# Optimization experiments

Hardware: AMD Instinct MI355X
Metric: run time of the kernel (lower is better)

## Reference

```python
import jax, jax.numpy as jnp
import numpy as np

H = 768
NH = 12
HD = H // NH  # 64
WINDOW = 64  # module's self.window_size; band keeps |i-j| <= WINDOW//2


def setup_inputs() -> dict:
    key = jax.random.key(0)
    ks = jax.random.split(key, 9)
    s = 0.02
    return {
        "hidden_states": jax.random.normal(ks[0], (4, 2048, H), dtype=jnp.float32),
        "Wq": jax.random.normal(ks[1], (H, H), dtype=jnp.float32) * s,
        "bq": jnp.zeros((H,), dtype=jnp.float32),
        "Wk": jax.random.normal(ks[2], (H, H), dtype=jnp.float32) * s,
        "bk": jnp.zeros((H,), dtype=jnp.float32),
        "Wv": jax.random.normal(ks[3], (H, H), dtype=jnp.float32) * s,
        "bv": jnp.zeros((H,), dtype=jnp.float32),
        "Wo": jax.random.normal(ks[4], (H, H), dtype=jnp.float32) * s,
        "bo": jnp.zeros((H,), dtype=jnp.float32),
    }


def _attn(hidden_states, Wq, bq, Wk, bk, Wv, bv, Wo, bo):
    B, S, _ = hidden_states.shape
    # projections (torch Linear uses y = x @ W.T + b; here W is stored already transposed)
    q = (hidden_states @ Wq + bq).reshape(B, S, NH, HD).transpose(0, 2, 1, 3)
    k = (hidden_states @ Wk + bk).reshape(B, S, NH, HD).transpose(0, 2, 1, 3)
    v = (hidden_states @ Wv + bv).reshape(B, S, NH, HD).transpose(0, 2, 1, 3)
    # dense scores [B, NH, S, S], faithful to the original O(S^2) computation
    scores = jnp.einsum("bhqd,bhkd->bhqk", q, k) / jnp.sqrt(jnp.float32(HD))
    # sliding-window band mask: keep j in [i - W//2, i + W//2]
    i = jnp.arange(S)[:, None]
    j = jnp.arange(S)[None, :]
    band = jnp.abs(i - j) <= (WINDOW // 2)
    scores = jnp.where(band[None, None, :, :], scores, jnp.float32(-1e9))
    probs = jax.nn.softmax(scores, axis=-1)
    ctx = jnp.einsum("bhqk,bhkd->bhqd", probs, v)
    ctx = ctx.transpose(0, 2, 1, 3).reshape(B, S, H)
    return ctx @ Wo + bo


def reference(hidden_states, Wq, bq, Wk, bk, Wv, bv, Wo, bo):
    return _attn(hidden_states, Wq, bq, Wk, bk, Wv, bv, Wo, bo)
```

## Files before the change

kernel.cpp:

```cpp
#include <hip/hip_runtime.h>
#include <hip/hip_bf16.h>

#define NHEAD 12
#define HD 64
#define SEQ 2048
#define NB 4
#define HDIM 768
#define MTOT (NB * SEQ)

typedef float f32x4 __attribute__((ext_vector_type(4)));
typedef float f32x16 __attribute__((ext_vector_type(16)));
typedef short s16x8 __attribute__((ext_vector_type(8)));
typedef unsigned short u16x8 __attribute__((ext_vector_type(8)));

__device__ inline unsigned short f2bf(float f) {
    union { float f; unsigned u; } v; v.f = f;
    unsigned r = v.u + 0x7fffu + ((v.u >> 16) & 1u);
    return (unsigned short)(r >> 16);
}
__device__ inline float bf2f(unsigned short u) {
    union { unsigned u; float f; } v; v.u = ((unsigned)u) << 16;
    return v.f;
}
__device__ inline unsigned pack_bf2(float a, float b) {
    return (unsigned)f2bf(a) | ((unsigned)f2bf(b) << 16);
}
__device__ inline s16x8 mk_frag(uint2 lo, uint2 hi) {
    union { unsigned u[4]; s16x8 v; } r;
    r.u[0] = lo.x; r.u[1] = lo.y; r.u[2] = hi.x; r.u[3] = hi.y;
    return r.v;
}

#define MFMA(acc, a, b) \
    acc = __builtin_amdgcn_mfma_f32_16x16x32_bf16((a), (b), (acc), 0, 0, 0)
#define MFMA32(acc, a, b) \
    acc = __builtin_amdgcn_mfma_f32_32x32x16_bf16((a), (b), (acc), 0, 0, 0)

__global__ __launch_bounds__(256) void x_convert(
    const float* __restrict__ X, unsigned short* __restrict__ Xb)
{
    const int i = (blockIdx.x * 256 + threadIdx.x) * 8;
    float4 a = *(const float4*)(X + i);
    float4 b = *(const float4*)(X + i + 4);
    ushort4 wa, wb;
    wa.x = f2bf(a.x); wa.y = f2bf(a.y); wa.z = f2bf(a.z); wa.w = f2bf(a.w);
    wb.x = f2bf(b.x); wb.y = f2bf(b.y); wb.z = f2bf(b.z); wb.w = f2bf(b.w);
    *(ushort4*)(Xb + i) = wa;
    *(ushort4*)(Xb + i + 4) = wb;
}

__global__ __launch_bounds__(256) void w_transpose(
    const float* __restrict__ Wq, const float* __restrict__ Wk,
    const float* __restrict__ Wv, const float* __restrict__ Wo,
    unsigned short* __restrict__ Wt, unsigned short* __restrict__ Wot)
{
    __shared__ __align__(16) unsigned short ts[64][68];
    const int z = blockIdx.z;
    const float* W = (z == 0) ? Wq : (z == 1) ? Wk : (z == 2) ? Wv : Wo;
    unsigned short* D = (z < 3) ? (Wt + (size_t)z * HDIM * HDIM) : Wot;
    const int k0 = blockIdx.x * 64, n0 = blockIdx.y * 64;
    const int t = threadIdx.x;
    const int kr = (t >> 4) * 4;
    const int nc = (t & 15) * 4;
    #pragma unroll
    for (int r = 0; r < 4; r++) {
        float4 v = *(const float4*)(W + (size_t)(k0 + kr + r) * HDIM + n0 + nc);
        ushort4 w;
        w.x = f2bf(v.x); w.y = f2bf(v.y); w.z = f2bf(v.z); w.w = f2bf(v.w);
        *(ushort4*)&ts[kr + r][nc] = w;
    }
    __syncthreads();
    const int nr = t >> 2;
    const int kc = (t & 3) * 16;
    #pragma unroll
    for (int j4 = 0; j4 < 4; j4++) {
        ushort4 w;
        w.x = ts[kc + j4 * 4 + 0][nr];
        w.y = ts[kc + j4 * 4 + 1][nr];
        w.z = ts[kc + j4 * 4 + 2][nr];
        w.w = ts[kc + j4 * 4 + 3][nr];
        *(ushort4*)(D + (size_t)(n0 + nr) * HDIM + k0 + kc + j4 * 4) = w;
    }
}

#define LDP 72

template<int MODE>
__global__ __launch_bounds__(256) void gemm_kernel(
    const unsigned short* __restrict__ A,
    const unsigned short* __restrict__ Bt,
    const float* __restrict__ bias0, const float* __restrict__ bias1,
    const float* __restrict__ bias2,
    unsigned short* __restrict__ Qb, unsigned short* __restrict__ Kb,
    unsigned short* __restrict__ Vb, float* __restrict__ out)
{
    __shared__ __align__(16) unsigned short As[128 * LDP];
    __shared__ __align__(16) unsigned short Bs[128 * LDP];

    const int t = threadIdx.x;
    const int lane = t & 63;
    const int wid = t >> 6;
    const int wm = wid >> 1, wn = wid & 1;
    const int l31 = lane & 31;
    const int lh = lane >> 5;

    const int m0 = blockIdx.y * 128;
    const int n0 = blockIdx.x * 128;

    f32x16 acc[2][2] = {};

    for (int k0 = 0; k0 < HDIM; k0 += 64) {
        u16x8 ra[4], rb[4];
        #pragma unroll
        for (int i = 0; i < 4; i++) {
            const int f = i * 256 + t;
            const int row = f >> 3, c8 = f & 7;
            ra[i] = *(const u16x8*)(A  + (size_t)(m0 + row) * HDIM + k0 + c8 * 8);
            rb[i] = *(const u16x8*)(Bt + (size_t)(n0 + row) * HDIM + k0 + c8 * 8);
        }
        __syncthreads();
        #pragma unroll
        for (int i = 0; i < 4; i++) {
            const int f = i * 256 + t;
            const int row = f >> 3, c8 = f & 7;
            *(u16x8*)(As + row * LDP + c8 * 8) = ra[i];
            *(u16x8*)(Bs + row * LDP + c8 * 8) = rb[i];
        }
        __syncthreads();

        #pragma unroll
        for (int kv = 0; kv < 4; kv++) {
            const int co = kv * 16 + lh * 8;
            s16x8 a0 = *(const s16x8*)(As + (wm * 64 +      l31) * LDP + co);
            s16x8 a1 = *(const s16x8*)(As + (wm * 64 + 32 + l31) * LDP + co);
            s16x8 b0 = *(const s16x8*)(Bs + (wn * 64 +      l31) * LDP + co);
            s16x8 b1 = *(const s16x8*)(Bs + (wn * 64 + 32 + l31) * LDP + co);
            MFMA32(acc[0][0], a0, b0);
            MFMA32(acc[0][1], a0, b1);
            MFMA32(acc[1][0], a1, b0);
            MFMA32(acc[1][1], a1, b1);
        }
    }

    if (MODE == 0) {
        const int z = n0 / HDIM;
        const float* bias = (z == 0) ? bias0 : (z == 1) ? bias1 : bias2;
        const float scale = (z == 0) ? 0.125f : 1.0f;
        unsigned short* dst = (z == 0) ? Qb : (z == 1) ? Kb : Vb;
        #pragma unroll
        for (int fm = 0; fm < 2; fm++) {
            #pragma unroll
            for (int fn = 0; fn < 2; fn++) {
                const int coll = (n0 - z * HDIM) + wn * 64 + fn * 32 + l31;
                const float bc = bias[coll];
                const int h = coll >> 6, d = coll & 63;
                #pragma unroll
                for (int reg = 0; reg < 16; reg++) {
                    const int rowD = (reg & 3) + 8 * (reg >> 2) + 4 * lh;
                    const int m = m0 + wm * 64 + fm * 32 + rowD;
                    const int b = m >> 11, s = m & (SEQ - 1);
                    const size_t idx = (z == 2)
                        ? ((((size_t)b * NHEAD + h) * HD + d) * SEQ + s)
                        : ((((size_t)b * NHEAD + h) * SEQ + s) * HD + d);
                    dst[idx] = f2bf((acc[fm][fn][reg] + bc) * scale);
                }
            }
        }
    } else {
        #pragma unroll
        for (int fm = 0; fm < 2; fm++) {
            #pragma unroll
            for (int fn = 0; fn < 2; fn++) {
                const int col = n0 + wn * 64 + fn * 32 + l31;
                const float bc = bias0[col];
                #pragma unroll
                for (int reg = 0; reg < 16; reg++) {
                    const int rowD = (reg & 3) + 8 * (reg >> 2) + 4 * lh;
                    const int m = m0 + wm * 64 + fm * 32 + rowD;
                    out[(size_t)m * HDIM + col] = acc[fm][fn][reg] + bc;
                }
            }
        }
    }
}

__global__ __launch_bounds__(512) void attn_mfma(
    const unsigned short* __restrict__ Qb, const unsigned short* __restrict__ Kb,
    const unsigned short* __restrict__ Vtg, unsigned short* __restrict__ Cb)
{
    __shared__ __align__(16) unsigned short Ks[192][72];
    __shared__ __align__(16) unsigned short Qs[128][72];
    __shared__ __align__(16) unsigned short Vs[64][208];

    const int t = threadIdx.x;
    const int lane = t & 63;
    const int wq = t >> 6;
    const int woff = wq * 16;
    const int g = lane >> 4, r16 = lane & 15;
    const int q0 = blockIdx.x * 128;
    const int bh = blockIdx.y;
    const int b = bh / NHEAD, h = bh - b * NHEAD;
    const size_t base  = (size_t)bh * SEQ * HD;
    const size_t vbase = (size_t)bh * HD * SEQ;
    const int kstart = q0 - 32;
    const bool interior = (kstart >= 0) && (kstart + 191 < SEQ);

    if (t < 384) {
        const int row = t >> 1, c0 = (t & 1) * 32;
        const int s = kstart + row;
        if (s >= 0 && s < SEQ) {
            const unsigned short* src = Kb + base + (size_t)s * HD + c0;
            #pragma unroll
            for (int j = 0; j < 4; j++)
                *(u16x8*)&Ks[row][c0 + 8 * j] = *(const u16x8*)(src + 8 * j);
        } else {
            const u16x8 z = {};
            #pragma unroll
            for (int j = 0; j < 4; j++)
                *(u16x8*)&Ks[row][c0 + 8 * j] = z;
        }
    }
    {
        const int row = t >> 2, c0 = (t & 3) * 16;
        const unsigned short* src = Qb + base + (size_t)(q0 + row) * HD + c0;
        *(u16x8*)&Qs[row][c0] = *(const u16x8*)src;
        *(u16x8*)&Qs[row][c0 + 8] = *(const u16x8*)(src + 8);
    }
    {
        const int row = t >> 3, c0 = (t & 7) * 24;
        const unsigned short* src = Vtg + vbase + (size_t)row * SEQ + kstart + c0;
        if (interior) {
            #pragma unroll
            for (int j = 0; j < 3; j++)
                *(u16x8*)&Vs[row][c0 + 8 * j] = *(const u16x8*)(src + 8 * j);
        } else {
            for (int e = 0; e < 24; e++) {
                const int s = kstart + c0 + e;
                Vs[row][c0 + e] = (s >= 0 && s < SEQ) ? src[e] : (unsigned short)0;
            }
        }
        if (t < 128) {
            const u16x8 z = {};
            *(u16x8*)&Vs[t >> 1][192 + (t & 1) * 8] = z;
        }
    }
    __syncthreads();

    s16x8 qf[2];
    {
        const unsigned short* p = &Qs[woff + r16][0];
        #pragma unroll
        for (int c = 0; c < 2; c++)
            qf[c] = mk_frag(*(const uint2*)(p + c * 32 + 4 * g),
                            *(const uint2*)(p + c * 32 + 16 + 4 * g));
    }
    f32x4 sacc[5] = {};
    #pragma unroll
    for (int mf = 0; mf < 5; mf++) {
        const unsigned short* p = &Ks[woff + mf * 16 + r16][0];
        #pragma unroll
        for (int c = 0; c < 2; c++) {
            s16x8 kf = mk_frag(*(const uint2*)(p + c * 32 + 4 * g),
                               *(const uint2*)(p + c * 32 + 16 + 4 * g));
            MFMA(sacc[mf], kf, qf[c]);
        }
    }

    float mx = -1e30f;
    #pragma unroll
    for (int mf = 0; mf < 5; mf++) {
        #pragma unroll
        for (int r = 0; r < 4; r++) {
            const int rel = mf * 16 + 4 * g + r - r16;
            const int sg = kstart + woff + mf * 16 + 4 * g + r;
            const bool ok = (rel >= 0) && (rel <= 64) && (sg >= 0) && (sg < SEQ);
            const float v = ok ? sacc[mf][r] : -1e30f;
            sacc[mf][r] = v;
            mx = fmaxf(mx, v);
        }
    }
    mx = fmaxf(mx, __shfl_xor(mx, 16));
    mx = fmaxf(mx, __shfl_xor(mx, 32));
    float l = 0.f;
    #pragma unroll
    for (int mf = 0; mf < 5; mf++) {
        #pragma unroll
        for (int r = 0; r < 4; r++) {
            const float e = __expf(sacc[mf][r] - mx);
            sacc[mf][r] = e;
            l += e;
        }
    }
    l += __shfl_xor(l, 16);
    l += __shfl_xor(l, 32);
    const float inv = 1.f / l;

    s16x8 pf[3];
    #pragma unroll
    for (int c = 0; c < 3; c++) {
        union { unsigned u[4]; s16x8 v; } pv;
        pv.u[0] = pack_bf2(sacc[2 * c][0] * inv, sacc[2 * c][1] * inv);
        pv.u[1] = pack_bf2(sacc[2 * c][2] * inv, sacc[2 * c][3] * inv);
        if (c < 2) {
            pv.u[2] = pack_bf2(sacc[2 * c + 1][0] * inv, sacc[2 * c + 1][1] * inv);
            pv.u[3] = pack_bf2(sacc[2 * c + 1][2] * inv, sacc[2 * c + 1][3] * inv);
        } else {
            pv.u[2] = 0; pv.u[3] = 0;
        }
        pf[c] = pv.v;
    }

    f32x4 cacc[4] = {};
    #pragma unroll
    for (int nf = 0; nf < 4; nf++) {
        const unsigned short* p = &Vs[nf * 16 + r16][woff];
        #pragma unroll
        for (int c = 0; c < 3; c++) {
            s16x8 vf = mk_frag(*(const uint2*)(p + c * 32 + 4 * g),
                               *(const uint2*)(p + c * 32 + 16 + 4 * g));
            MFMA(cacc[nf], pf[c], vf);
        }
    }

    #pragma unroll
    for (int nf = 0; nf < 4; nf++) {
        #pragma unroll
        for (int r = 0; r < 4; r++) {
            const int ql = woff + 4 * g + r;
            const int d = nf * 16 + r16;
            Cb[(((size_t)b * SEQ + q0 + ql) * NHEAD + h) * HD + d] = f2bf(cacc[nf][r]);
        }
    }
}

extern "C" void kernel_launch(void* const* d_in, const int* in_sizes, int n_in,
                              void* d_out, int out_size, void* d_ws, size_t ws_size,
                              hipStream_t stream)
{
    const float* X  = (const float*)d_in[0];
    const float* Wq = (const float*)d_in[1];
    const float* bq = (const float*)d_in[2];
    const float* Wk = (const float*)d_in[3];
    const float* bk = (const float*)d_in[4];
    const float* Wv = (const float*)d_in[5];
    const float* bv = (const float*)d_in[6];
    const float* Wo = (const float*)d_in[7];
    const float* bo = (const float*)d_in[8];
    float* out = (float*)d_out;

    char* ws = (char*)d_ws;
    unsigned short* Xb  = (unsigned short*)ws;
    unsigned short* Cb  = Xb;
    unsigned short* Vt  = (unsigned short*)(ws + 12582912);
    unsigned short* Wtp = (unsigned short*)(ws + 25165824);
    unsigned short* Wot = (unsigned short*)(ws + 28704768);
    unsigned short* Qb  = (unsigned short*)d_out;
    unsigned short* Kb  = (unsigned short*)((char*)d_out + 12582912);

    x_convert<<<dim3(3072), 256, 0, stream>>>(X, Xb);
    w_transpose<<<dim3(12, 12, 4), 256, 0, stream>>>(Wq, Wk, Wv, Wo, Wtp, Wot);
    gemm_kernel<0><<<dim3(18, 64), 256, 0, stream>>>(Xb, Wtp, bq, bk, bv, Qb, Kb, Vt, nullptr);
    attn_mfma<<<dim3(16, 48), 512, 0, stream>>>(Qb, Kb, Vt, Cb);
    gemm_kernel<1><<<dim3(6, 64), 256, 0, stream>>>(Cb, Wot, bo, nullptr, nullptr,
                                                    nullptr, nullptr, nullptr, out);
}
```

Measured before the change: 123.4 us.

## Load GEMM tiles directly into LDS with XOR-swizzled layout

Replaces the register-staged global-to-LDS copy in the projection GEMMs with direct global_load_lds transfers. Padded LDS rows give way to an XOR swizzle (applied on the global source addresses) to avoid bank conflicts on the MFMA fragment reads. The grid is also transposed so M tiles vary fastest, which changes the order in which weight tiles are reused across blocks. This cuts VGPR pressure and LDS store instructions, but still has no double buffering, and correctness depends on how the lanes of each wave map into the LDS destination.

New measurement: 111.8 us. -9.4%, faster.

```diff
diff --git a/kernel.cpp b/kernel.cpp
--- a/kernel.cpp
+++ b/kernel.cpp
@@ -29,6 +29,11 @@
     union { unsigned u[4]; s16x8 v; } r;
     r.u[0] = lo.x; r.u[1] = lo.y; r.u[2] = hi.x; r.u[3] = hi.y;
     return r.v;
+}
+__device__ inline void gload_lds16(const unsigned short* g, void* lds_base) {
+    __builtin_amdgcn_global_load_lds(
+        (const __attribute__((address_space(1))) void*)g,
+        (__attribute__((address_space(3))) void*)lds_base, 16, 0, 0);
 }
 
 #define MFMA(acc, a, b) \
@@ -83,8 +88,6 @@
     }
 }
 
-#define LDP 72
-
 template<int MODE>
 __global__ __launch_bounds__(256) void gemm_kernel(
     const unsigned short* __restrict__ A,
@@ -94,8 +97,8 @@
     unsigned short* __restrict__ Qb, unsigned short* __restrict__ Kb,
     unsigned short* __restrict__ Vb, float* __restrict__ out)
 {
-    __shared__ __align__(16) unsigned short As[128 * LDP];
-    __shared__ __align__(16) unsigned short Bs[128 * LDP];
+    __shared__ __align__(16) unsigned short As[128 * 64];
+    __shared__ __align__(16) unsigned short Bs[128 * 64];
 
     const int t = threadIdx.x;
     const int lane = t & 63;
@@ -104,37 +107,41 @@
     const int l31 = lane & 31;
     const int lh = lane >> 5;
 
-    const int m0 = blockIdx.y * 128;
-    const int n0 = blockIdx.x * 128;
+    const int m0 = blockIdx.x * 128;
+    const int n0 = blockIdx.y * 128;
+
+    int srow[4], scol[4];
+    #pragma unroll
+    for (int i = 0; i < 4; i++) {
+        const int p = i * 4096 + t * 16;
+        const int row = p >> 7;
+        const int cb = p & 127;
+        srow[i] = row;
+        scol[i] = (cb ^ ((row & 7) << 4)) >> 1;
+    }
 
     f32x16 acc[2][2] = {};
 
     for (int k0 = 0; k0 < HDIM; k0 += 64) {
-        u16x8 ra[4], rb[4];
-        #pragma unroll
-        for (int i = 0; i < 4; i++) {
-            const int f = i * 256 + t;
-            const int row = f >> 3, c8 = f & 7;
-            ra[i] = *(const u16x8*)(A  + (size_t)(m0 + row) * HDIM + k0 + c8 * 8);
-            rb[i] = *(const u16x8*)(Bt + (size_t)(n0 + row) * HDIM + k0 + c8 * 8);
-        }
         __syncthreads();
         #pragma unroll
-        for (int i = 0; i < 4; i++) {
-            const int f = i * 256 + t;
-            const int row = f >> 3, c8 = f & 7;
-            *(u16x8*)(As + row * LDP + c8 * 8) = ra[i];
-            *(u16x8*)(Bs + row * LDP + c8 * 8) = rb[i];
-        }
+        for (int i = 0; i < 4; i++)
+            gload_lds16(A + (size_t)(m0 + srow[i]) * HDIM + k0 + scol[i],
+                        (char*)As + i * 4096 + wid * 1024);
+        #pragma unroll
+        for (int i = 0; i < 4; i++)
+            gload_lds16(Bt + (size_t)(n0 + srow[i]) * HDIM + k0 + scol[i],
+                        (char*)Bs + i * 4096 + wid * 1024);
         __syncthreads();
 
+        const int sw = (l31 & 7) << 4;
         #pragma unroll
         for (int kv = 0; kv < 4; kv++) {
-            const int co = kv * 16 + lh * 8;
-            s16x8 a0 = *(const s16x8*)(As + (wm * 64 +      l31) * LDP + co);
-            s16x8 a1 = *(const s16x8*)(As + (wm * 64 + 32 + l31) * LDP + co);
-            s16x8 b0 = *(const s16x8*)(Bs + (wn * 64 +      l31) * LDP + co);
-            s16x8 b1 = *(const s16x8*)(Bs + (wn * 64 + 32 + l31) * LDP + co);
+            const int cb = (kv * 32 + lh * 16) ^ sw;
+            s16x8 a0 = *(const s16x8*)((const char*)As + (wm * 64 +      l31) * 128 + cb);
+            s16x8 a1 = *(const s16x8*)((const char*)As + (wm * 64 + 32 + l31) * 128 + cb);
+            s16x8 b0 = *(const s16x8*)((const char*)Bs + (wn * 64 +      l31) * 128 + cb);
+            s16x8 b1 = *(const s16x8*)((const char*)Bs + (wn * 64 + 32 + l31) * 128 + cb);
             MFMA32(acc[0][0], a0, b0);
             MFMA32(acc[0][1], a0, b1);
             MFMA32(acc[1][0], a1, b0);
@@ -359,8 +366,8 @@
 
     x_convert<<<dim3(3072), 256, 0, stream>>>(X, Xb);
     w_transpose<<<dim3(12, 12, 4), 256, 0, stream>>>(Wq, Wk, Wv, Wo, Wtp, Wot);
-    gemm_kernel<0><<<dim3(18, 64), 256, 0, stream>>>(Xb, Wtp, bq, bk, bv, Qb, Kb, Vt, nullptr);
+    gemm_kernel<0><<<dim3(64, 18), 256, 0, stream>>>(Xb, Wtp, bq, bk, bv, Qb, Kb, Vt, nullptr);
     attn_mfma<<<dim3(16, 48), 512, 0, stream>>>(Qb, Kb, Vt, Cb);
-    gemm_kernel<1><<<dim3(6, 64), 256, 0, stream>>>(Cb, Wot, bo, nullptr, nullptr,
+    gemm_kernel<1><<<dim3(64, 6), 256, 0, stream>>>(Cb, Wot, bo, nullptr, nullptr,
                                                     nullptr, nullptr, nullptr, out);
 }
```
